# Performance work log

Measured on AMD Instinct MI355X. Metric: run time of the kernel, lower is better.

The kernel has to match this reference:

```python
import jax, jax.numpy as jnp
import numpy as np

B, H, W, C = 1, 64, 64, 256
NH = 8
K = 7


def setup_inputs() -> dict:
    key = jax.random.key(0)
    ks = jax.random.split(key, 6)
    x = jax.random.normal(ks[0], (B, H, W, C), dtype=jnp.float32)
    # torch nn.Linear weights are [out, in]
    qkv_w = jax.random.normal(ks[1], (3 * C, C), dtype=jnp.float32) * 0.02
    qkv_b = jnp.zeros((3 * C,), dtype=jnp.float32)
    proj_w = jax.random.normal(ks[2], (C, C), dtype=jnp.float32) * 0.02
    proj_b = jnp.zeros((C,), dtype=jnp.float32)
    # relative position bias table: [num_heads, 2K-1, 2K-1]
    rpb = jax.random.normal(ks[3], (NH, 2 * K - 1, 2 * K - 1), dtype=jnp.float32) * 0.02
    return {"x": x, "qkv_w": qkv_w, "qkv_b": qkv_b, "proj_w": proj_w,
            "proj_b": proj_b, "rpb": rpb}


def _neighbor_idx(n, k):
    # clamped window starts (NATTEN semantics): each query sees exactly k neighbors
    start = jnp.clip(jnp.arange(n) - k // 2, 0, n - k)  # [n]
    return start[:, None] + jnp.arange(k)[None, :]       # [n, k]


def reference(x, qkv_w, qkv_b, proj_w, proj_b, rpb):
    b, h, w, c = x.shape
    nh = rpb.shape[0]
    k = (rpb.shape[1] + 1) // 2
    hd = c // nh
    scale = hd ** -0.5

    qkv = x @ qkv_w.T + qkv_b                              # [b,h,w,3c]
    qkv = qkv.reshape(b, h, w, 3, nh, hd)
    qkv = jnp.transpose(qkv, (3, 0, 4, 1, 2, 5))           # [3,b,nh,h,w,hd]
    q, kk, v = qkv[0], qkv[1], qkv[2]

    ni = _neighbor_idx(h, k)                               # [h,k]
    nj = _neighbor_idx(w, k)                               # [w,k]

    # gather neighborhood keys/values: [b,nh,h,k,w,k,hd]
    k_nb = kk[:, :, ni][:, :, :, :, nj]
    v_nb = v[:, :, ni][:, :, :, :, nj]

    # attention logits over the k x k window
    attn = jnp.einsum('bnijd,bniajcd->bnijac', q * scale, k_nb)  # [b,nh,h,w,k,k]

    # relative position bias: index = (neighbor - query) + (k-1)
    bi = ni - jnp.arange(h)[:, None] + (k - 1)             # [h,k]
    bj = nj - jnp.arange(w)[:, None] + (k - 1)             # [w,k]
    bias = rpb[:, bi][:, :, :, bj]                         # [nh,h,k,w,k]
    attn = attn + jnp.transpose(bias, (0, 1, 3, 2, 4))[None]

    attn = jax.nn.softmax(attn.reshape(b, nh, h, w, k * k), axis=-1)
    attn = attn.reshape(b, nh, h, w, k, k)

    out = jnp.einsum('bnijac,bniajcd->bnijd', attn, v_nb)  # [b,nh,h,w,hd]
    out = jnp.transpose(out, (0, 2, 3, 1, 4)).reshape(b, h, w, c)
    out = out @ proj_w.T + proj_b
    return out
```

## Files before the change

### kernel.cpp

```cpp
#include <hip/hip_runtime.h>
#include <math.h>

#define HH 64
#define WW 64
#define CC 256
#define NHEAD 8
#define HD 32
#define KW 7
#define NPIX (HH * WW)

#define HALO_H 10
#define HALO_W 14
#define NROWH (HALO_H * HALO_W)
#define KROW 40
#define PST 51

typedef _Float16 half2v __attribute__((ext_vector_type(2)));
typedef _Float16 half8v __attribute__((ext_vector_type(8)));
typedef __fp16 fp16x2 __attribute__((ext_vector_type(2)));
typedef float float4v __attribute__((ext_vector_type(4)));

__device__ __forceinline__ unsigned pkrtz(float lo, float hi) {
  union { fp16x2 h; unsigned u; } c;
  c.h = __builtin_amdgcn_cvt_pkrtz(lo, hi);
  return c.u;
}
__device__ __forceinline__ half2v h2(unsigned u) {
  union { unsigned u; half2v h; } c;
  c.u = u;
  return c.h;
}
__device__ __forceinline__ unsigned h2u(half2v h) {
  union { half2v h; unsigned u; } c;
  c.h = h;
  return c.u;
}
__device__ __forceinline__ ushort f2h(float f) {
  union { _Float16 h; ushort u; } c;
  c.h = (_Float16)f;
  return c.u;
}

template <int N, int BM, int BN, bool ABF, bool OB>
__global__ __launch_bounds__(256) void gemm5h(
    const void* __restrict__ Ap, const float* __restrict__ Bw,
    const float* __restrict__ bias, void* __restrict__ Cd) {
  constexpr int SEGA = BM / 32;
  constexpr int SEGB = BN / 32;
  constexpr int MF = BM / 32;
  constexpr int NF = BN / 32;

  __shared__ ushort As[2][BM * 64];
  __shared__ ushort Bs[2][BN * 64];

  const int t = threadIdx.x;
  const int lane = t & 63;
  const int wave = t >> 6;
  const int bm = blockIdx.x * BM;
  const int bn = blockIdx.y * BN;

  const float*  Aw = (const float*)Ap;
  const ushort* Ab = (const ushort*)Ap;

  float fA[2][SEGA][8];
  float fB[2][SEGB][8];
  uint4 wA[2][SEGA];

#define LOADA(c, s)                                                            \
  {                                                                            \
    _Pragma("unroll") for (int sa = 0; sa < SEGA; ++sa) {                      \
      const int seg = sa * 256 + t;                                            \
      const int row = seg >> 3;                                                \
      const int q8 = seg & 7;                                                  \
      if (ABF) {                                                               \
        wA[s][sa] =                                                            \
            *(const uint4*)(Ab + (size_t)(bm + row) * 256 + (c) * 64 + q8 * 8);\
      } else {                                                                 \
        const float* p_ = Aw + (size_t)(bm + row) * 256 + (c) * 64 + q8 * 8;   \
        *(float4*)&fA[s][sa][0] = *(const float4*)(p_);                        \
        *(float4*)&fA[s][sa][4] = *(const float4*)(p_ + 4);                    \
      }                                                                        \
    }                                                                          \
  }

#define LOADB(c, s)                                                            \
  {                                                                            \
    _Pragma("unroll") for (int sb = 0; sb < SEGB; ++sb) {                      \
      const int seg = sb * 256 + t;                                            \
      const int row = seg >> 3;                                                \
      const int q8 = seg & 7;                                                  \
      const float* p_ = Bw + (size_t)(bn + row) * 256 + (c) * 64 + q8 * 8;     \
      *(float4*)&fB[s][sb][0] = *(const float4*)(p_);                          \
      *(float4*)&fB[s][sb][4] = *(const float4*)(p_ + 4);                      \
    }                                                                          \
  }

#define WRITEC(b, s)                                                           \
  {                                                                            \
    _Pragma("unroll") for (int sa = 0; sa < SEGA; ++sa) {                      \
      const int seg = sa * 256 + t;                                            \
      const int row = seg >> 3;                                                \
      const int q8 = seg & 7;                                                  \
      const int lin = row * 128 + q8 * 16;                                     \
      const int sw = (row & 7) << 4;                                           \
      uint4 w_;                                                                \
      if (ABF) {                                                               \
        w_ = wA[s][sa];                                                        \
      } else {                                                                 \
        w_.x = pkrtz(fA[s][sa][0], fA[s][sa][1]);                              \
        w_.y = pkrtz(fA[s][sa][2], fA[s][sa][3]);                              \
        w_.z = pkrtz(fA[s][sa][4], fA[s][sa][5]);                              \
        w_.w = pkrtz(fA[s][sa][6], fA[s][sa][7]);                              \
      }                                                                        \
      *(uint4*)((char*)As[b] + (lin ^ sw)) = w_;                               \
    }                                                                          \
    _Pragma("unroll") for (int sb = 0; sb < SEGB; ++sb) {                      \
      const int seg = sb * 256 + t;                                            \
      const int row = seg >> 3;                                                \
      const int q8 = seg & 7;                                                  \
      const int lin = row * 128 + q8 * 16;                                     \
      const int sw = (row & 7) << 4;                                           \
      uint4 w_;                                                                \
      w_.x = pkrtz(fB[s][sb][0], fB[s][sb][1]);                                \
      w_.y = pkrtz(fB[s][sb][2], fB[s][sb][3]);                                \
      w_.z = pkrtz(fB[s][sb][4], fB[s][sb][5]);                                \
      w_.w = pkrtz(fB[s][sb][6], fB[s][sb][7]);                                \
      *(uint4*)((char*)Bs[b] + (lin ^ sw)) = w_;                               \
    }                                                                          \
  }

  const int wr = (wave >> 1) * (BM / 2);
  const int wc = (wave & 1) * (BN / 2);
  const int lrow = lane & 15;
  const int lkb = (lane >> 4) * 16;

  float4v acc[MF][NF];
#pragma unroll
  for (int mf = 0; mf < MF; ++mf)
#pragma unroll
    for (int nf = 0; nf < NF; ++nf) acc[mf][nf] = (float4v){0.f, 0.f, 0.f, 0.f};

  LOADA(0, 0); LOADB(0, 0);
  WRITEC(0, 0);
  LOADA(1, 1); LOADB(1, 1);
  __syncthreads();

#pragma unroll
  for (int c = 0; c < 4; ++c) {
    if (c < 3) WRITEC((c + 1) & 1, (c + 1) & 1);
    if (c < 2) { LOADA(c + 2, c & 1); LOADB(c + 2, c & 1); }
    const char* Al = (const char*)As[c & 1];
    const char* Bl = (const char*)Bs[c & 1];
#pragma unroll
    for (int ks = 0; ks < 2; ++ks) {
      half8v af[MF], bfr[NF];
#pragma unroll
      for (int mf = 0; mf < MF; ++mf) {
        const int row = wr + mf * 16 + lrow;
        const int ad = row * 128 + ks * 64 + lkb;
        af[mf] = *(const half8v*)(Al + (ad ^ ((row & 7) << 4)));
      }
#pragma unroll
      for (int nf = 0; nf < NF; ++nf) {
        const int row = wc + nf * 16 + lrow;
        const int bd = row * 128 + ks * 64 + lkb;
        bfr[nf] = *(const half8v*)(Bl + (bd ^ ((row & 7) << 4)));
      }
#pragma unroll
      for (int mf = 0; mf < MF; ++mf)
#pragma unroll
        for (int nf = 0; nf < NF; ++nf)
          acc[mf][nf] = __builtin_amdgcn_mfma_f32_16x16x32_f16(
              af[mf], bfr[nf], acc[mf][nf], 0, 0, 0);
    }
    if (c < 3) __syncthreads();
  }
#undef LOADA
#undef LOADB
#undef WRITEC

#pragma unroll
  for (int mf = 0; mf < MF; ++mf) {
#pragma unroll
    for (int nf = 0; nf < NF; ++nf) {
      const int n = bn + wc + nf * 16 + lrow;
      const float bv = bias[n];
      const int m0 = bm + wr + mf * 16 + (lane >> 4) * 4;
      if (OB) {
        ushort* C = (ushort*)Cd;
#pragma unroll
        for (int rr = 0; rr < 4; ++rr)
          C[(size_t)(m0 + rr) * N + n] = f2h(acc[mf][nf][rr] + bv);
      } else {
        float* C = (float*)Cd;
#pragma unroll
        for (int rr = 0; rr < 4; ++rr)
          C[(size_t)(m0 + rr) * N + n] = acc[mf][nf][rr] + bv;
      }
    }
  }
}

__global__ __launch_bounds__(256) void natten6(
    const ushort* __restrict__ qkv, const float* __restrict__ rpb,
    ushort* __restrict__ aout) {
  __shared__ ushort Ks[NROWH * KROW];
  __shared__ ushort Vs[NROWH * KROW];
  __shared__ float Ps[32][PST];
  __shared__ float Rs[169];

  const int head = blockIdx.y;
  const int tile = blockIdx.x;
  const int i0 = (tile >> 3) * 4, j0 = (tile & 7) * 8;
  const int hs = min(max(i0 - 3, 0), HH - HALO_H);
  const int ws = min(max(j0 - 3, 0), WW - HALO_W);
  const int t = threadIdx.x;

  if (t < 169) Rs[t] = rpb[head * 169 + t];

  {
    const int lane4 = t & 3;
    const int r0 = t >> 2;
#pragma unroll
    for (int it = 0; it < 5; ++it) {
      const int task = it * 64 + r0;
      if (task < 2 * NROWH) {
        const int mat = task >= NROWH;
        const int row = task - mat * NROWH;
        const int hr = row / HALO_W;
        const int hc = row - hr * HALO_W;
        const int g = (hs + hr) * WW + (ws + hc);
        const uint4 val = *(const uint4*)(qkv + (size_t)g * 768 + 256 + mat * 256 +
                                          head * HD + lane4 * 8);
        ushort* dst = (mat ? Vs : Ks) + row * KROW + lane4 * 8;
        *(uint4*)dst = val;
      }
    }
  }
  __syncthreads();

  const int p = t >> 3;
  const int tp = t & 7;
  const int i = i0 + (p >> 3), j = j0 + (p & 7);
  const int si = min(max(i - 3, 0), HH - KW);
  const int sj = min(max(j - 3, 0), WW - KW);
  const int lr0 = si - hs, lc0 = sj - ws;
  const int bi0 = si - i + (KW - 1);
  const int bj0 = sj - j + (KW - 1);

  unsigned qpk[16];
  {
    const ushort* qp = qkv + (size_t)(i * WW + j) * 768 + head * HD;
#pragma unroll
    for (int z = 0; z < 4; ++z) {
      const uint4 u = *(const uint4*)(qp + z * 8);
      qpk[z * 4 + 0] = u.x;
      qpk[z * 4 + 1] = u.y;
      qpk[z * 4 + 2] = u.z;
      qpk[z * 4 + 3] = u.w;
    }
  }

  const float scale = 0.17677669529663687f;

  const int nbeg = tp * 7;
  float lg[7];
#pragma unroll
  for (int z = 0; z < 7; ++z) lg[z] = -INFINITY;

#pragma unroll
  for (int z = 0; z < 7; ++z) {
    const int n = nbeg + z;
    if (n < KW * KW) {
      const int a = n / KW;
      const int c = n - a * KW;
      const int krow = (lr0 + a) * HALO_W + (lc0 + c);
      const ushort* kp = Ks + krow * KROW;
      half2v h0 = {0.f, 0.f}, h1 = {0.f, 0.f};
#pragma unroll
      for (int zz = 0; zz < 4; ++zz) {
        const uint4 k4 = *(const uint4*)(kp + zz * 8);
        h0 += h2(qpk[zz * 4 + 0]) * h2(k4.x);
        h1 += h2(qpk[zz * 4 + 1]) * h2(k4.y);
        h0 += h2(qpk[zz * 4 + 2]) * h2(k4.z);
        h1 += h2(qpk[zz * 4 + 3]) * h2(k4.w);
      }
      const float s = (float)h0[0] + (float)h0[1] + (float)h1[0] + (float)h1[1];
      lg[z] = s * scale + Rs[(bi0 + a) * 13 + (bj0 + c)];
    }
  }

  float ssum = 0.f;
#pragma unroll
  for (int z = 0; z < 7; ++z) {
    const float e = __expf(lg[z]);
    lg[z] = e;
    ssum += e;
  }
  ssum += __shfl_xor(ssum, 1, 8);
  ssum += __shfl_xor(ssum, 2, 8);
  ssum += __shfl_xor(ssum, 4, 8);
  const float inv = 1.f / ssum;

#pragma unroll
  for (int z = 0; z < 7; ++z) {
    const int n = nbeg + z;
    if (n < KW * KW) Ps[p][n] = lg[z] * inv;
  }
  __syncthreads();

  const int half = tp >> 2;
  const int d0 = (tp & 3) * 8;
  half2v o0 = {0.f, 0.f}, o1 = {0.f, 0.f}, o2 = {0.f, 0.f}, o3 = {0.f, 0.f};
#pragma unroll
  for (int z = 0; z < 25; ++z) {
    const int n = half * 25 + z;
    if (n < KW * KW) {
      const int a = n / KW;
      const int c = n - a * KW;
      const float pr = Ps[p][n];
      const half2v ph = h2(pkrtz(pr, pr));
      const int vrow = (lr0 + a) * HALO_W + (lc0 + c);
      const uint4 v4 = *(const uint4*)(Vs + vrow * KROW + d0);
      o0 += ph * h2(v4.x);
      o1 += ph * h2(v4.y);
      o2 += ph * h2(v4.z);
      o3 += ph * h2(v4.w);
    }
  }
  o0 += h2(__shfl_xor(h2u(o0), 4, 8));
  o1 += h2(__shfl_xor(h2u(o1), 4, 8));
  o2 += h2(__shfl_xor(h2u(o2), 4, 8));
  o3 += h2(__shfl_xor(h2u(o3), 4, 8));

  if ((tp & 4) == 0) {
    uint4 st;
    st.x = h2u(o0); st.y = h2u(o1); st.z = h2u(o2); st.w = h2u(o3);
    *(uint4*)(aout + (size_t)(i * WW + j) * CC + head * HD + d0) = st;
  }
}

extern "C" void kernel_launch(void* const* d_in, const int* in_sizes, int n_in,
                              void* d_out, int out_size, void* d_ws, size_t ws_size,
                              hipStream_t stream) {
  const float* x      = (const float*)d_in[0];
  const float* qkv_w  = (const float*)d_in[1];
  const float* qkv_b  = (const float*)d_in[2];
  const float* proj_w = (const float*)d_in[3];
  const float* proj_b = (const float*)d_in[4];
  const float* rpb    = (const float*)d_in[5];
  float* out = (float*)d_out;

  ushort* qkvh  = (ushort*)d_ws;
  ushort* aouth = qkvh + 3145728;

  gemm5h<768, 32, 64, false, true><<<dim3(128, 12), 256, 0, stream>>>(
      x, qkv_w, qkv_b, qkvh);

  natten6<<<dim3(128, NHEAD), 256, 0, stream>>>(qkvh, rpb, aouth);

  gemm5h<256, 32, 32, true, false><<<dim3(128, 8), 256, 0, stream>>>(
      aouth, proj_w, proj_b, out);
}
```

Baseline: 29.13 us.

## Rewrite neighborhood attention with MFMA over padded halo slabs

The attention kernel now computes QK logits and PV products with 16x16x32 fp16 MFMA instructions instead of scalar packed-half dot products. Each wave handles a 2x8 pixel strip and evaluates scores against an 8x16 padded halo slab, then masks out-of-window entries. V is stored transposed in shared memory, and probabilities are exchanged through shuffles rather than a shared buffer and second barrier. Tiles are enlarged to 8x8 pixels with half as many blocks. The cost is extra wasted work on the masked padding and transposed scalar LDS stores.

```diff
diff --git a/kernel.cpp b/kernel.cpp
--- a/kernel.cpp
+++ b/kernel.cpp
@@ -9,11 +9,8 @@
 #define KW 7
 #define NPIX (HH * WW)
 
-#define HALO_H 10
-#define HALO_W 14
-#define NROWH (HALO_H * HALO_W)
-#define KROW 40
-#define PST 51
+#define KR 40
+#define VTS 232
 
 typedef _Float16 half2v __attribute__((ext_vector_type(2)));
 typedef _Float16 half8v __attribute__((ext_vector_type(8)));
@@ -23,16 +20,6 @@
 __device__ __forceinline__ unsigned pkrtz(float lo, float hi) {
   union { fp16x2 h; unsigned u; } c;
   c.h = __builtin_amdgcn_cvt_pkrtz(lo, hi);
-  return c.u;
-}
-__device__ __forceinline__ half2v h2(unsigned u) {
-  union { unsigned u; half2v h; } c;
-  c.u = u;
-  return c.h;
-}
-__device__ __forceinline__ unsigned h2u(half2v h) {
-  union { half2v h; unsigned u; } c;
-  c.h = h;
   return c.u;
 }
 __device__ __forceinline__ ushort f2h(float f) {
@@ -201,142 +188,147 @@
   }
 }
 
-__global__ __launch_bounds__(256) void natten6(
+__global__ __launch_bounds__(256) void natten7(
     const ushort* __restrict__ qkv, const float* __restrict__ rpb,
     ushort* __restrict__ aout) {
-  __shared__ ushort Ks[NROWH * KROW];
-  __shared__ ushort Vs[NROWH * KROW];
-  __shared__ float Ps[32][PST];
+  __shared__ ushort Ks[224 * KR];
+  __shared__ ushort Vt[32 * VTS];
   __shared__ float Rs[169];
 
   const int head = blockIdx.y;
   const int tile = blockIdx.x;
-  const int i0 = (tile >> 3) * 4, j0 = (tile & 7) * 8;
-  const int hs = min(max(i0 - 3, 0), HH - HALO_H);
-  const int ws = min(max(j0 - 3, 0), WW - HALO_W);
+  const int i0 = (tile >> 3) * 8, j0 = (tile & 7) * 8;
+  const int hs = min(max(i0 - 3, 0), HH - 14);
+  const int ws = min(max(j0 - 3, 0), WW - 14);
   const int t = threadIdx.x;
+  const int l = t & 63;
+  const int wv = t >> 6;
 
   if (t < 169) Rs[t] = rpb[head * 169 + t];
 
-  {
-    const int lane4 = t & 3;
-    const int r0 = t >> 2;
-#pragma unroll
-    for (int it = 0; it < 5; ++it) {
-      const int task = it * 64 + r0;
-      if (task < 2 * NROWH) {
-        const int mat = task >= NROWH;
-        const int row = task - mat * NROWH;
-        const int hr = row / HALO_W;
-        const int hc = row - hr * HALO_W;
-        const int g = (hs + hr) * WW + (ws + hc);
-        const uint4 val = *(const uint4*)(qkv + (size_t)g * 768 + 256 + mat * 256 +
-                                          head * HD + lane4 * 8);
-        ushort* dst = (mat ? Vs : Ks) + row * KROW + lane4 * 8;
-        *(uint4*)dst = val;
-      }
+  if (t < 112) {
+    const int ent2 = t >> 2;
+    const int hr = ent2 >> 1, hc = 14 + (ent2 & 1);
+    const uint4 z = {0u, 0u, 0u, 0u};
+    *(uint4*)(Ks + (hr * 16 + hc) * KR + (t & 3) * 8) = z;
+  }
+#pragma unroll
+  for (int it = 0; it < 2; ++it) {
+    const int task = it * 256 + t;
+    const int d = task >> 4, hr = task & 15;
+    if (hr < 14) *(unsigned*)(Vt + d * VTS + hr * 16 + 14) = 0u;
+  }
+
+#pragma unroll
+  for (int s = 0; s < 4; ++s) {
+    if (t < 196) {
+      const int hr = (t * 2341) >> 15;
+      const int hc = t - hr * 14;
+      const int g = (hs + hr) * WW + (ws + hc);
+      const int col = hr * 16 + hc;
+      const uint4 kv = *(const uint4*)(qkv + (size_t)g * 768 + 256 + head * HD + s * 8);
+      *(uint4*)(Ks + col * KR + s * 8) = kv;
+      const uint4 vv = *(const uint4*)(qkv + (size_t)g * 768 + 512 + head * HD + s * 8);
+      const int d0 = s * 8;
+      Vt[(d0 + 0) * VTS + col] = (ushort)(vv.x);
+      Vt[(d0 + 1) * VTS + col] = (ushort)(vv.x >> 16);
+      Vt[(d0 + 2) * VTS + col] = (ushort)(vv.y);
+      Vt[(d0 + 3) * VTS + col] = (ushort)(vv.y >> 16);
+      Vt[(d0 + 4) * VTS + col] = (ushort)(vv.z);
+      Vt[(d0 + 5) * VTS + col] = (ushort)(vv.z >> 16);
+      Vt[(d0 + 6) * VTS + col] = (ushort)(vv.w);
+      Vt[(d0 + 7) * VTS + col] = (ushort)(vv.w >> 16);
     }
   }
   __syncthreads();
 
-  const int p = t >> 3;
-  const int tp = t & 7;
-  const int i = i0 + (p >> 3), j = j0 + (p & 7);
-  const int si = min(max(i - 3, 0), HH - KW);
-  const int sj = min(max(j - 3, 0), WW - KW);
-  const int lr0 = si - hs, lc0 = sj - ws;
-  const int bi0 = si - i + (KW - 1);
-  const int bj0 = sj - j + (KW - 1);
-
-  unsigned qpk[16];
-  {
-    const ushort* qp = qkv + (size_t)(i * WW + j) * 768 + head * HD;
-#pragma unroll
-    for (int z = 0; z < 4; ++z) {
-      const uint4 u = *(const uint4*)(qp + z * 8);
-      qpk[z * 4 + 0] = u.x;
-      qpk[z * 4 + 1] = u.y;
-      qpk[z * 4 + 2] = u.z;
-      qpk[z * 4 + 3] = u.w;
-    }
-  }
-
+  const int strip_i0 = i0 + wv * 2;
+  const int lg = l >> 4;
+  const int l15 = l & 15;
+
+  const int pi = strip_i0 + (l15 >> 3);
+  const int pj = j0 + (l15 & 7);
+  const int si = min(max(pi - 3, 0), HH - KW);
+  const int sj = min(max(pj - 3, 0), WW - KW);
+  const int si_min = min(max(strip_i0 - 3, 0), HH - KW);
+  const int slab0 = min(si_min - hs, 6);
+
+  const half8v qf = *(const half8v*)(qkv + (size_t)(pi * WW + pj) * 768 +
+                                     head * HD + lg * 8);
+
+  float4v s8[8];
+  const float4v zz = {0.f, 0.f, 0.f, 0.f};
+#pragma unroll
+  for (int g = 0; g < 8; ++g) {
+    const int ent = (slab0 + g) * 16 + l15;
+    const half8v kf = *(const half8v*)(Ks + ent * KR + lg * 8);
+    s8[g] = __builtin_amdgcn_mfma_f32_16x16x32_f16(kf, qf, zz, 0, 0, 0);
+  }
+
+  const int lr0 = si - hs;
+  const int lc0 = sj - ws;
+  const int abase = slab0 - lr0;
+  const int rowb = ((si - pi + 6) + abase) * 13 + (sj - pj + 6) - lc0;
   const float scale = 0.17677669529663687f;
 
-  const int nbeg = tp * 7;
-  float lg[7];
-#pragma unroll
-  for (int z = 0; z < 7; ++z) lg[z] = -INFINITY;
-
-#pragma unroll
-  for (int z = 0; z < 7; ++z) {
-    const int n = nbeg + z;
-    if (n < KW * KW) {
-      const int a = n / KW;
-      const int c = n - a * KW;
-      const int krow = (lr0 + a) * HALO_W + (lc0 + c);
-      const ushort* kp = Ks + krow * KROW;
-      half2v h0 = {0.f, 0.f}, h1 = {0.f, 0.f};
-#pragma unroll
-      for (int zz = 0; zz < 4; ++zz) {
-        const uint4 k4 = *(const uint4*)(kp + zz * 8);
-        h0 += h2(qpk[zz * 4 + 0]) * h2(k4.x);
-        h1 += h2(qpk[zz * 4 + 1]) * h2(k4.y);
-        h0 += h2(qpk[zz * 4 + 2]) * h2(k4.z);
-        h1 += h2(qpk[zz * 4 + 3]) * h2(k4.w);
-      }
-      const float s = (float)h0[0] + (float)h0[1] + (float)h1[0] + (float)h1[1];
-      lg[z] = s * scale + Rs[(bi0 + a) * 13 + (bj0 + c)];
-    }
-  }
-
+  float e8[8][4];
   float ssum = 0.f;
 #pragma unroll
-  for (int z = 0; z < 7; ++z) {
-    const float e = __expf(lg[z]);
-    lg[z] = e;
-    ssum += e;
-  }
-  ssum += __shfl_xor(ssum, 1, 8);
-  ssum += __shfl_xor(ssum, 2, 8);
-  ssum += __shfl_xor(ssum, 4, 8);
+  for (int g = 0; g < 8; ++g) {
+    const int a = abase + g;
+    const bool va = (unsigned)a < 7u;
+    const int idxg = min(max(rowb + g * 13, 0), 153);
+#pragma unroll
+    for (int r = 0; r < 4; ++r) {
+      const int hc = lg * 4 + r;
+      const bool vc = (unsigned)(hc - lc0) < 7u;
+      const float ev = __expf(fmaf(s8[g][r], scale, Rs[idxg + hc]));
+      const float em = (va && vc) ? ev : 0.f;
+      e8[g][r] = em;
+      ssum += em;
+    }
+  }
+  ssum += __shfl_xor(ssum, 16);
+  ssum += __shfl_xor(ssum, 32);
   const float inv = 1.f / ssum;
 
-#pragma unroll
-  for (int z = 0; z < 7; ++z) {
-    const int n = nbeg + z;
-    if (n < KW * KW) Ps[p][n] = lg[z] * inv;
-  }
-  __syncthreads();
-
-  const int half = tp >> 2;
-  const int d0 = (tp & 3) * 8;
-  half2v o0 = {0.f, 0.f}, o1 = {0.f, 0.f}, o2 = {0.f, 0.f}, o3 = {0.f, 0.f};
-#pragma unroll
-  for (int z = 0; z < 25; ++z) {
-    const int n = half * 25 + z;
-    if (n < KW * KW) {
-      const int a = n / KW;
-      const int c = n - a * KW;
-      const float pr = Ps[p][n];
-      const half2v ph = h2(pkrtz(pr, pr));
-      const int vrow = (lr0 + a) * HALO_W + (lc0 + c);
-      const uint4 v4 = *(const uint4*)(Vs + vrow * KROW + d0);
-      o0 += ph * h2(v4.x);
-      o1 += ph * h2(v4.y);
-      o2 += ph * h2(v4.z);
-      o3 += ph * h2(v4.w);
-    }
-  }
-  o0 += h2(__shfl_xor(h2u(o0), 4, 8));
-  o1 += h2(__shfl_xor(h2u(o1), 4, 8));
-  o2 += h2(__shfl_xor(h2u(o2), 4, 8));
-  o3 += h2(__shfl_xor(h2u(o3), 4, 8));
-
-  if ((tp & 4) == 0) {
-    uint4 st;
-    st.x = h2u(o0); st.y = h2u(o1); st.z = h2u(o2); st.w = h2u(o3);
-    *(uint4*)(aout + (size_t)(i * WW + j) * CC + head * HD + d0) = st;
+  unsigned Wp[8][2];
+#pragma unroll
+  for (int g = 0; g < 8; ++g) {
+    Wp[g][0] = pkrtz(e8[g][0] * inv, e8[g][1] * inv);
+    Wp[g][1] = pkrtz(e8[g][2] * inv, e8[g][3] * inv);
+  }
+
+  float4v o[2] = {zz, zz};
+#pragma unroll
+  for (int ks = 0; ks < 4; ++ks) {
+    unsigned F[4];
+#pragma unroll
+    for (int f = 0; f < 4; ++f) {
+      const int src = l15 + (((lg & 1) * 2 + (f >> 1)) << 4);
+      const unsigned va = __shfl(Wp[2 * ks][f & 1], src);
+      const unsigned vb = __shfl(Wp[2 * ks + 1][f & 1], src);
+      F[f] = (lg >> 1) ? vb : va;
+    }
+    union { unsigned u[4]; half8v h; } pf;
+    pf.u[0] = F[0]; pf.u[1] = F[1]; pf.u[2] = F[2]; pf.u[3] = F[3];
+#pragma unroll
+    for (int nf = 0; nf < 2; ++nf) {
+      const int dim = l15 + nf * 16;
+      const half8v vf = *(const half8v*)(Vt + dim * VTS + slab0 * 16 +
+                                         ks * 32 + lg * 8);
+      o[nf] = __builtin_amdgcn_mfma_f32_16x16x32_f16(pf.h, vf, o[nf], 0, 0, 0);
+    }
+  }
+
+#pragma unroll
+  for (int r = 0; r < 4; ++r) {
+    const int pxo = lg * 4 + r;
+    const int oi = strip_i0 + (pxo >> 3);
+    const int oj = j0 + (pxo & 7);
+    ushort* op = aout + (size_t)(oi * WW + oj) * CC + head * HD + l15;
+    op[0]  = f2h(o[0][r]);
+    op[16] = f2h(o[1][r]);
   }
 }
 
@@ -357,7 +349,7 @@
   gemm5h<768, 32, 64, false, true><<<dim3(128, 12), 256, 0, stream>>>(
       x, qkv_w, qkv_b, qkvh);
 
-  natten6<<<dim3(128, NHEAD), 256, 0, stream>>>(qkvh, rpb, aouth);
+  natten7<<<dim3(64, NHEAD), 256, 0, stream>>>(qkvh, rpb, aouth);
 
   gemm5h<256, 32, 32, true, false><<<dim3(128, 8), 256, 0, stream>>>(
       aouth, proj_w, proj_b, out);
```

After: 25.40 us. 1.15x faster.
